# Performance work log

Hardware: AMD Instinct MI355X
Metric: run time of the kernel (lower is better)

Reference implementation:

```python
import jax, jax.numpy as jnp
import numpy as np

B, N, F, D, DB, C = 1024, 200000, 32, 128, 256, 96


def _ln(x, g, b, eps=1e-5):
    m = x.mean(-1, keepdims=True)
    v = ((x - m) ** 2).mean(-1, keepdims=True)
    return (x - m) / jnp.sqrt(v + eps) * g + b


def setup_inputs() -> dict:
    key = jax.random.key(0)
    ks = jax.random.split(key, 24)
    s = 0.05
    inp = {
        'x_num': jax.random.normal(ks[0], (B, F), jnp.float32),
        'cand_x_num': jax.random.normal(ks[1], (N, F), jnp.float32),
        'cand_y': jax.random.normal(ks[2], (N,), jnp.float32),
        'W_in': jax.random.normal(ks[3], (F, D), jnp.float32) * s,
        'b_in': jnp.zeros((D,), jnp.float32),
        'enc_w1': jax.random.normal(ks[4], (D, DB), jnp.float32) * s,
        'enc_b1': jnp.zeros((DB,), jnp.float32),
        'enc_w2': jax.random.normal(ks[5], (DB, D), jnp.float32) * s,
        'enc_b2': jnp.zeros((D,), jnp.float32),
        'ln_mix_g': jnp.ones((D,), jnp.float32),
        'ln_mix_b': jnp.zeros((D,), jnp.float32),
        'K_w': jax.random.normal(ks[6], (D, D), jnp.float32) * s,
        'K_b': jnp.zeros((D,), jnp.float32),
        'lab_w': jax.random.normal(ks[7], (1, D), jnp.float32) * s,
        'lab_b': jnp.zeros((D,), jnp.float32),
        'T_w1': jax.random.normal(ks[8], (D, DB), jnp.float32) * s,
        'T_b1': jnp.zeros((DB,), jnp.float32),
        'T_w2': jax.random.normal(ks[9], (DB, D), jnp.float32) * s,  # no bias
        'pred_ln_g': jnp.ones((D,), jnp.float32),
        'pred_ln_b': jnp.zeros((D,), jnp.float32),
        'pred_w1': jax.random.normal(ks[10], (D, DB), jnp.float32) * s,
        'pred_b1': jnp.zeros((DB,), jnp.float32),
        'pred_w2': jax.random.normal(ks[11], (DB, D), jnp.float32) * s,
        'pred_b2': jnp.zeros((D,), jnp.float32),
        'head_ln_g': jnp.ones((D,), jnp.float32),
        'head_ln_b': jnp.zeros((D,), jnp.float32),
        'head_w': jax.random.normal(ks[12], (D, 1), jnp.float32) * s,
        'head_b': jnp.zeros((1,), jnp.float32),
        'context_size': C,
    }
    return inp


def _forward(x_num, cand_x_num, cand_y, W_in, b_in, enc_w1, enc_b1, enc_w2, enc_b2,
             ln_mix_g, ln_mix_b, K_w, K_b, lab_w, lab_b, T_w1, T_b1, T_w2,
             pred_ln_g, pred_ln_b, pred_w1, pred_b1, pred_w2, pred_b2,
             head_ln_g, head_ln_b, head_w, head_b, context_size):
    def enc(z):
        h = z @ W_in + b_in                                   # [*, D]
        h = h + (jax.nn.relu(h @ enc_w1 + enc_b1) @ enc_w2 + enc_b2)
        k = _ln(h, ln_mix_g, ln_mix_b) @ K_w + K_b
        return h, k

    cand_k = enc(cand_x_num)[1]                               # [N, D]
    x, k = enc(x_num)                                         # [B, D]

    # brute-force kNN: negative squared L2 via matmul + square sums
    k2 = (k * k).sum(-1, keepdims=True)                       # [B, 1]
    ck2 = (cand_k * cand_k).sum(-1)                           # [N]
    sims = 2.0 * (k @ cand_k.T) - k2 - ck2[None, :]           # [B, N]
    _, idx = jax.lax.top_k(sims, context_size)                # [B, C]

    context_k = cand_k[idx]                                   # [B, C, D]
    sim_c = 2.0 * jnp.einsum('bd,bcd->bc', k, context_k) - k2 - (context_k ** 2).sum(-1)
    probs = jax.nn.softmax(sim_c, axis=-1)                    # [B, C]

    ctx_y = cand_y[idx][..., None] @ lab_w + lab_b            # [B, C, D]
    diff = k[:, None, :] - context_k                          # [B, C, D]
    vals = ctx_y + jax.nn.relu(diff @ T_w1 + T_b1) @ T_w2     # [B, C, D]
    context_x = jnp.einsum('bc,bcd->bd', probs, vals)         # [B, D]

    x = x + context_x
    h = _ln(x, pred_ln_g, pred_ln_b)
    x = x + (jax.nn.relu(h @ pred_w1 + pred_b1) @ pred_w2 + pred_b2)
    out = jax.nn.relu(_ln(x, head_ln_g, head_ln_b)) @ head_w + head_b
    return out                                                # [B, 1]


def reference(x_num, cand_x_num, cand_y, W_in, b_in, enc_w1, enc_b1, enc_w2, enc_b2,
              ln_mix_g, ln_mix_b, K_w, K_b, lab_w, lab_b, T_w1, T_b1, T_w2,
              pred_ln_g, pred_ln_b, pred_w1, pred_b1, pred_w2, pred_b2,
              head_ln_g, head_ln_b, head_w, head_b, context_size):
    return _forward(x_num, cand_x_num, cand_y, W_in, b_in, enc_w1, enc_b1, enc_w2, enc_b2,
                    ln_mix_g, ln_mix_b, K_w, K_b, lab_w, lab_b, T_w1, T_b1, T_w2,
                    pred_ln_g, pred_ln_b, pred_w1, pred_b1, pred_w2, pred_b2,
                    head_ln_g, head_ln_b, head_w, head_b, context_size)
```

## Files before the change

kernel.cpp:

```cpp
#include <hip/hip_runtime.h>
#include <hip/hip_bf16.h>

#define NC 200000
#define NCP 200064
#define NCT 1563
#define CGR 196
#define BB 1024
#define DD 128
#define DBH 256
#define CS 96
#define CAPS 8192
#define RSLOT6 6

typedef __attribute__((ext_vector_type(8))) short bf16x8;
typedef __attribute__((ext_vector_type(4))) float f32x4;

#define LDH 136
#define LDU 264
#define LDT 136

__device__ inline uint4 pack8(const float4 a, const float4 b) {
  union { __hip_bfloat16 h[8]; uint4 v; } r;
  r.h[0] = __float2bfloat16(a.x); r.h[1] = __float2bfloat16(a.y);
  r.h[2] = __float2bfloat16(a.z); r.h[3] = __float2bfloat16(a.w);
  r.h[4] = __float2bfloat16(b.x); r.h[5] = __float2bfloat16(b.y);
  r.h[6] = __float2bfloat16(b.z); r.h[7] = __float2bfloat16(b.w);
  return r.v;
}

__device__ inline unsigned encf(float v) {
  unsigned b = __float_as_uint(v);
  return (b & 0x80000000u) ? ~b : (b | 0x80000000u);
}
__device__ inline float decf(unsigned u) {
  return __uint_as_float((u & 0x80000000u) ? (u ^ 0x80000000u) : ~u);
}
__device__ inline unsigned long long mkkey(float v, int idx) {
  unsigned u = encf(v);
  return (((unsigned long long)(~u)) << 32) | (unsigned)idx;
}

__global__ __launch_bounds__(256) void k_prep(const float* __restrict__ w1,
                                              const float* __restrict__ w2,
                                              const float* __restrict__ kw,
                                              const float* __restrict__ tw1,
                                              __hip_bfloat16* __restrict__ w1t,
                                              __hip_bfloat16* __restrict__ w2t,
                                              __hip_bfloat16* __restrict__ kwt,
                                              __hip_bfloat16* __restrict__ tw1t) {
  const int i = blockIdx.x * 256 + threadIdx.x;
  if (i < 32768) {
    const int u = i >> 7, j = i & 127;
    w1t[i] = __float2bfloat16(w1[j * DBH + u]);
    tw1t[i] = __float2bfloat16(tw1[j * DBH + u]);
  }
  if (i < 32768) {
    const int d = i >> 8, u = i & 255;
    w2t[i] = __float2bfloat16(w2[u * DD + d]);
  }
  if (i < 16384) {
    const int d = i >> 7, j = i & 127;
    kwt[i] = __float2bfloat16(kw[j * DD + d]);
  }
}

__global__ __launch_bounds__(256) void k_pad(__hip_bfloat16* __restrict__ ckb16,
                                             float* __restrict__ ck2) {
  const int i = blockIdx.x * 256 + threadIdx.x;
  if (i < (NCP - NC) * DD) ckb16[(size_t)NC * DD + i] = __float2bfloat16(0.f);
  if (i < (NCP - NC)) ck2[NC + i] = 1e9f;
}

__global__ __launch_bounds__(256) void k_clear(unsigned* __restrict__ rowmaxP,
                                               int* __restrict__ cnt) {
  const int i = blockIdx.x * 256 + threadIdx.x;
  if (i < BB * 16) { rowmaxP[i] = 0u; cnt[i] = 0; }
}

__global__ __launch_bounds__(256) void k_e1(const float* __restrict__ X,
                                            const float* __restrict__ W,
                                            const float* __restrict__ bias,
                                            float* __restrict__ H) {
  __shared__ float Xs[32 * 32];
  const int tid = threadIdx.x;
  const int r0 = blockIdx.x * 32;
  ((float4*)Xs)[tid] = ((const float4*)(X + (size_t)r0 * 32))[tid];
  __syncthreads();
  const int d0 = tid & 63;
  const int rh = tid >> 6;
  float acc0[8], acc1[8];
  const float b0 = bias[d0], b1 = bias[d0 + 64];
#pragma unroll
  for (int r = 0; r < 8; ++r) { acc0[r] = b0; acc1[r] = b1; }
#pragma unroll
  for (int k4 = 0; k4 < 8; ++k4) {
    float w0[4], w1[4];
#pragma unroll
    for (int kk = 0; kk < 4; ++kk) {
      w0[kk] = W[(k4 * 4 + kk) * DD + d0];
      w1[kk] = W[(k4 * 4 + kk) * DD + d0 + 64];
    }
#pragma unroll
    for (int r = 0; r < 8; ++r) {
      float4 x4 = ((const float4*)(Xs + (rh * 8 + r) * 32))[k4];
      acc0[r] += x4.x * w0[0] + x4.y * w0[1] + x4.z * w0[2] + x4.w * w0[3];
      acc1[r] += x4.x * w1[0] + x4.y * w1[1] + x4.z * w1[2] + x4.w * w1[3];
    }
  }
#pragma unroll
  for (int r = 0; r < 8; ++r) {
    const size_t row = (size_t)(r0 + rh * 8 + r);
    H[row * DD + d0] = acc0[r];
    H[row * DD + d0 + 64] = acc1[r];
  }
}

__global__ __launch_bounds__(256) void k_e23m(float* __restrict__ H,
                                              const __hip_bfloat16* __restrict__ W1t,
                                              const float* __restrict__ B1,
                                              const __hip_bfloat16* __restrict__ W2t,
                                              const float* __restrict__ B2) {
  __shared__ __hip_bfloat16 Hs[64 * LDH];
  __shared__ __hip_bfloat16 Us[64 * LDU];
  const int tid = threadIdx.x;
  const int r0 = blockIdx.x * 64;
#pragma unroll
  for (int i = 0; i < 4; ++i) {
    const int e8 = i * 256 + tid;
    const int row = e8 >> 4, c8 = e8 & 15;
    const float* src = H + (size_t)(r0 + row) * DD + c8 * 8;
    float4 f0 = *(const float4*)(src);
    float4 f1 = *(const float4*)(src + 4);
    *(uint4*)(Hs + row * LDH + c8 * 8) = pack8(f0, f1);
  }
  __syncthreads();
  const int l = tid & 63, w = tid >> 6;
  const int lr = l & 15, lg = l >> 4;
  {
    f32x4 acc[4][4] = {};
#pragma unroll
    for (int kk = 0; kk < 4; ++kk) {
      bf16x8 a[4], b[4];
#pragma unroll
      for (int mi = 0; mi < 4; ++mi)
        a[mi] = *(const bf16x8*)(Hs + (mi * 16 + lr) * LDH + kk * 32 + lg * 8);
#pragma unroll
      for (int ni = 0; ni < 4; ++ni)
        b[ni] = *(const bf16x8*)(W1t + (size_t)(w * 64 + ni * 16 + lr) * DD + kk * 32 + lg * 8);
#pragma unroll
      for (int mi = 0; mi < 4; ++mi)
#pragma unroll
        for (int ni = 0; ni < 4; ++ni)
          acc[mi][ni] = __builtin_amdgcn_mfma_f32_16x16x32_bf16(a[mi], b[ni], acc[mi][ni], 0, 0, 0);
    }
#pragma unroll
    for (int ni = 0; ni < 4; ++ni) {
      const int col = w * 64 + ni * 16 + lr;
      const float bb = B1[col];
#pragma unroll
      for (int mi = 0; mi < 4; ++mi)
#pragma unroll
        for (int r = 0; r < 4; ++r) {
          const int row = mi * 16 + lg * 4 + r;
          Us[row * LDU + col] = __float2bfloat16(fmaxf(acc[mi][ni][r] + bb, 0.f));
        }
    }
  }
  __syncthreads();
  {
    f32x4 acc[4][2] = {};
#pragma unroll
    for (int kk = 0; kk < 8; ++kk) {
      bf16x8 a[4], b[2];
#pragma unroll
      for (int mi = 0; mi < 4; ++mi)
        a[mi] = *(const bf16x8*)(Us + (mi * 16 + lr) * LDU + kk * 32 + lg * 8);
#pragma unroll
      for (int ni = 0; ni < 2; ++ni)
        b[ni] = *(const bf16x8*)(W2t + (size_t)(w * 32 + ni * 16 + lr) * DBH + kk * 32 + lg * 8);
#pragma unroll
      for (int mi = 0; mi < 4; ++mi)
#pragma unroll
        for (int ni = 0; ni < 2; ++ni)
          acc[mi][ni] = __builtin_amdgcn_mfma_f32_16x16x32_bf16(a[mi], b[ni], acc[mi][ni], 0, 0, 0);
    }
#pragma unroll
    for (int ni = 0; ni < 2; ++ni) {
      const int col = w * 32 + ni * 16 + lr;
      const float bb = B2[col];
#pragma unroll
      for (int mi = 0; mi < 4; ++mi)
#pragma unroll
        for (int r = 0; r < 4; ++r) {
          const int row = mi * 16 + lg * 4 + r;
          const size_t g = (size_t)(r0 + row) * DD + col;
          H[g] = H[g] + acc[mi][ni][r] + bb;
        }
    }
  }
}

__global__ __launch_bounds__(256) void k_e4m(const float* __restrict__ H,
                                             const float* __restrict__ g,
                                             const float* __restrict__ bln,
                                             const __hip_bfloat16* __restrict__ Kwt,
                                             const float* __restrict__ Kb,
                                             float* __restrict__ Kout,
                                             __hip_bfloat16* __restrict__ Kb16,
                                             float* __restrict__ k2out) {
  __shared__ __hip_bfloat16 Ls[64 * LDH];
  __shared__ float k2s[64];
  const int tid = threadIdx.x;
  const int r0 = blockIdx.x * 64;
  if (tid < 64) k2s[tid] = 0.f;
  {
    const int row = tid >> 2, q = tid & 3;
    const float* hr = H + (size_t)(r0 + row) * DD + q * 32;
    float v[32];
#pragma unroll
    for (int i = 0; i < 8; ++i) {
      float4 f = ((const float4*)hr)[i];
      v[i * 4 + 0] = f.x; v[i * 4 + 1] = f.y; v[i * 4 + 2] = f.z; v[i * 4 + 3] = f.w;
    }
    float s = 0.f;
#pragma unroll
    for (int i = 0; i < 32; ++i) s += v[i];
    s += __shfl_xor(s, 1); s += __shfl_xor(s, 2);
    const float mean = s * (1.f / 128.f);
    float vs = 0.f;
#pragma unroll
    for (int i = 0; i < 32; ++i) { float d = v[i] - mean; vs += d * d; }
    vs += __shfl_xor(vs, 1); vs += __shfl_xor(vs, 2);
    const float rstd = 1.f / sqrtf(vs * (1.f / 128.f) + 1e-5f);
#pragma unroll
    for (int i = 0; i < 4; ++i) {
      float t[8];
#pragma unroll
      for (int j = 0; j < 8; ++j) {
        const int col = q * 32 + i * 8 + j;
        t[j] = (v[i * 8 + j] - mean) * rstd * g[col] + bln[col];
      }
      float4 f0 = {t[0], t[1], t[2], t[3]}, f1 = {t[4], t[5], t[6], t[7]};
      *(uint4*)(Ls + row * LDH + q * 32 + i * 8) = pack8(f0, f1);
    }
  }
  __syncthreads();
  const int l = tid & 63, w = tid >> 6;
  const int lr = l & 15, lg = l >> 4;
  f32x4 acc[4][2] = {};
#pragma unroll
  for (int kk = 0; kk < 4; ++kk) {
    bf16x8 a[4], b[2];
#pragma unroll
    for (int mi = 0; mi < 4; ++mi)
      a[mi] = *(const bf16x8*)(Ls + (mi * 16 + lr) * LDH + kk * 32 + lg * 8);
#pragma unroll
    for (int ni = 0; ni < 2; ++ni)
      b[ni] = *(const bf16x8*)(Kwt + (size_t)(w * 32 + ni * 16 + lr) * DD + kk * 32 + lg * 8);
#pragma unroll
    for (int mi = 0; mi < 4; ++mi)
#pragma unroll
      for (int ni = 0; ni < 2; ++ni)
        acc[mi][ni] = __builtin_amdgcn_mfma_f32_16x16x32_bf16(a[mi], b[ni], acc[mi][ni], 0, 0, 0);
  }
  float p[4][4];
#pragma unroll
  for (int mi = 0; mi < 4; ++mi)
#pragma unroll
    for (int r = 0; r < 4; ++r) p[mi][r] = 0.f;
#pragma unroll
  for (int ni = 0; ni < 2; ++ni) {
    const int col = w * 32 + ni * 16 + lr;
    const float kb = Kb[col];
#pragma unroll
    for (int mi = 0; mi < 4; ++mi)
#pragma unroll
      for (int r = 0; r < 4; ++r) {
        const float val = acc[mi][ni][r] + kb;
        const int row = mi * 16 + lg * 4 + r;
        const size_t gg = (size_t)(r0 + row) * DD + col;
        Kout[gg] = val;
        Kb16[gg] = __float2bfloat16(val);
        p[mi][r] += val * val;
      }
  }
#pragma unroll
  for (int mi = 0; mi < 4; ++mi)
#pragma unroll
    for (int r = 0; r < 4; ++r) {
      float t = p[mi][r];
      t += __shfl_xor(t, 1); t += __shfl_xor(t, 2);
      t += __shfl_xor(t, 4); t += __shfl_xor(t, 8);
      if (lr == 0) atomicAdd(&k2s[mi * 16 + lg * 4 + r], t);
    }
  __syncthreads();
  if (tid < 64) k2out[r0 + tid] = k2s[tid];
}

__global__ __launch_bounds__(256) void k_simsA(const __hip_bfloat16* __restrict__ A,
                                               const __hip_bfloat16* __restrict__ Bm,
                                               const float* __restrict__ ck2,
                                               unsigned* __restrict__ rowmaxP) {
  __shared__ __hip_bfloat16 As[128 * LDT];
  __shared__ __hip_bfloat16 Bs[128 * LDT];
  __shared__ float ck2s[128];
  __shared__ unsigned rmax_s[128];
  const int tid = threadIdx.x;
  const int bid = blockIdx.x;
  const int gq = bid >> 6, rem = bid & 63;
  const int rt = rem >> 3, xq = rem & 7;
  const int ct = gq * 8 + xq;
  if (ct >= NCT) return;
  const int m0 = rt * 128, n0 = ct * 128;
  if (tid < 128) { rmax_s[tid] = 0u; ck2s[tid] = 0.5f * ck2[n0 + tid]; }
  {
    const uint4* ga = (const uint4*)(A + (size_t)m0 * DD);
    const uint4* gb = (const uint4*)(Bm + (size_t)n0 * DD);
#pragma unroll
    for (int i = 0; i < 8; ++i) {
      const int e8 = i * 256 + tid;
      const int row = e8 >> 4, c8 = e8 & 15;
      *(uint4*)(As + row * LDT + c8 * 8) = ga[e8];
      *(uint4*)(Bs + row * LDT + c8 * 8) = gb[e8];
    }
  }
  __syncthreads();
  const int l = tid & 63, w = tid >> 6;
  const int wm = w >> 1, wn = w & 1;
  const int lr = l & 15, lg = l >> 4;
  f32x4 acc[4][4] = {};
#pragma unroll
  for (int kk = 0; kk < 4; ++kk) {
    bf16x8 a[4], b[4];
#pragma unroll
    for (int mi = 0; mi < 4; ++mi)
      a[mi] = *(const bf16x8*)(As + (wm * 64 + mi * 16 + lr) * LDT + kk * 32 + lg * 8);
#pragma unroll
    for (int ni = 0; ni < 4; ++ni)
      b[ni] = *(const bf16x8*)(Bs + (wn * 64 + ni * 16 + lr) * LDT + kk * 32 + lg * 8);
#pragma unroll
    for (int mi = 0; mi < 4; ++mi)
#pragma unroll
      for (int ni = 0; ni < 4; ++ni)
        acc[mi][ni] = __builtin_amdgcn_mfma_f32_16x16x32_bf16(a[mi], b[ni], acc[mi][ni], 0, 0, 0);
  }
  float vmax[4][4];
#pragma unroll
  for (int mi = 0; mi < 4; ++mi)
#pragma unroll
    for (int r = 0; r < 4; ++r) vmax[mi][r] = -1e30f;
#pragma unroll
  for (int ni = 0; ni < 4; ++ni) {
    const float c2 = ck2s[wn * 64 + ni * 16 + lr];
#pragma unroll
    for (int mi = 0; mi < 4; ++mi)
#pragma unroll
      for (int r = 0; r < 4; ++r)
        vmax[mi][r] = fmaxf(vmax[mi][r], acc[mi][ni][r] - c2);
  }
#pragma unroll
  for (int mi = 0; mi < 4; ++mi)
#pragma unroll
    for (int r = 0; r < 4; ++r) {
      float v = vmax[mi][r];
#pragma unroll
      for (int mk = 1; mk < 16; mk <<= 1) v = fmaxf(v, __shfl_xor(v, mk));
      if (lr == 0) atomicMax(&rmax_s[wm * 64 + mi * 16 + lg * 4 + r], encf(v));
    }
  __syncthreads();
  if (tid < 128) atomicMax(&rowmaxP[(m0 + tid) * 16], rmax_s[tid]);
}

__global__ __launch_bounds__(256) void k_simsB(const __hip_bfloat16* __restrict__ A,
                                               const __hip_bfloat16* __restrict__ Bm,
                                               const float* __restrict__ ck2,
                                               const unsigned* __restrict__ rowmaxP,
                                               unsigned long long* __restrict__ cand,
                                               int* __restrict__ cnt) {
  __shared__ __hip_bfloat16 As[128 * LDT];
  __shared__ __hip_bfloat16 Bs[128 * LDT];
  __shared__ float ck2s[128];
  __shared__ float cut_s[128];
  __shared__ unsigned long long loc[128][RSLOT6];
  __shared__ int lcnt[128];
  __shared__ int lbase[128];
  const int tid = threadIdx.x;
  const int bid = blockIdx.x;
  const int gq = bid >> 6, rem = bid & 63;
  const int rt = rem >> 3, xq = rem & 7;
  const int ct = gq * 8 + xq;
  if (ct >= NCT) return;
  const int m0 = rt * 128, n0 = ct * 128;
  if (tid < 128) {
    ck2s[tid] = 0.5f * ck2[n0 + tid];
    const float t = decf(rowmaxP[(m0 + tid) * 16]) - 7.0f;
    cut_s[tid] = t - (fabsf(t) + 8.0f) * 0.00390625f - 1e-5f;
    lcnt[tid] = 0;
  }
  {
    const uint4* ga = (const uint4*)(A + (size_t)m0 * DD);
    const uint4* gb = (const uint4*)(Bm + (size_t)n0 * DD);
#pragma unroll
    for (int i = 0; i < 8; ++i) {
      const int e8 = i * 256 + tid;
      const int row = e8 >> 4, c8 = e8 & 15;
      *(uint4*)(As + row * LDT + c8 * 8) = ga[e8];
      *(uint4*)(Bs + row * LDT + c8 * 8) = gb[e8];
    }
  }
  __syncthreads();
  const int l = tid & 63, w = tid >> 6;
  const int wm = w >> 1, wn = w & 1;
  const int lr = l & 15, lg = l >> 4;
  f32x4 acc[4][4] = {};
#pragma unroll
  for (int kk = 0; kk < 4; ++kk) {
    bf16x8 a[4], b[4];
#pragma unroll
    for (int mi = 0; mi < 4; ++mi)
      a[mi] = *(const bf16x8*)(As + (wm * 64 + mi * 16 + lr) * LDT + kk * 32 + lg * 8);
#pragma unroll
    for (int ni = 0; ni < 4; ++ni)
      b[ni] = *(const bf16x8*)(Bs + (wn * 64 + ni * 16 + lr) * LDT + kk * 32 + lg * 8);
#pragma unroll
    for (int mi = 0; mi < 4; ++mi)
#pragma unroll
      for (int ni = 0; ni < 4; ++ni)
        acc[mi][ni] = __builtin_amdgcn_mfma_f32_16x16x32_bf16(a[mi], b[ni], acc[mi][ni], 0, 0, 0);
  }
#pragma unroll
  for (int ni = 0; ni < 4; ++ni) {
    const int lcol = wn * 64 + ni * 16 + lr;
    const float c2 = ck2s[lcol];
    const int gcol = n0 + lcol;
#pragma unroll
    for (int mi = 0; mi < 4; ++mi)
#pragma unroll
      for (int r = 0; r < 4; ++r) {
        const int lrow = wm * 64 + mi * 16 + lg * 4 + r;
        const float x = acc[mi][ni][r] - c2;
        if (x >= cut_s[lrow]) {
          const float v = __bfloat162float(__float2bfloat16(x));
          const unsigned long long key = mkkey(v, gcol);
          const int q = atomicAdd(&lcnt[lrow], 1);
          if (q < RSLOT6) {
            loc[lrow][q] = key;
          } else {
            const int q2 = atomicAdd(&cnt[(m0 + lrow) * 16], 1);
            if (q2 < CAPS) cand[(size_t)(m0 + lrow) * CAPS + q2] = key;
          }
        }
      }
  }
  __syncthreads();
  if (tid < 128) {
    const int nres = lcnt[tid] < RSLOT6 ? lcnt[tid] : RSLOT6;
    lbase[tid] = atomicAdd(&cnt[(m0 + tid) * 16], nres);
  }
  __syncthreads();
  for (int e = tid; e < 128 * RSLOT6; e += 256) {
    const int rr = e / RSLOT6, s = e % RSLOT6;
    const int nres = lcnt[rr] < RSLOT6 ? lcnt[rr] : RSLOT6;
    if (s < nres) {
      const int pos = lbase[rr] + s;
      if (pos < CAPS) cand[(size_t)(m0 + rr) * CAPS + pos] = loc[rr][s];
    }
  }
}

__global__ __launch_bounds__(256) void k_sortB(const unsigned long long* __restrict__ cand,
                                               const int* __restrict__ cnt,
                                               int* __restrict__ idx_out) {
  __shared__ int wred[40][4];
  __shared__ int outl[128];
  __shared__ int outc_sh;
  const int tid = threadIdx.x;
  const int wid = tid >> 6, lane = tid & 63;
  const int row = blockIdx.x;
  int n = cnt[row * 16];
  if (n > CAPS) n = CAPS;

  unsigned v16l[32];
  int idl[32];
  {
    const unsigned long long* src = cand + (size_t)row * CAPS;
#pragma unroll
    for (int s = 0; s < 32; ++s) {
      const int i = tid + s * 256;
      if (i < n) {
        const unsigned long long k = src[i];
        v16l[s] = (~(unsigned)(k >> 32)) >> 16;
        idl[s] = (int)(k & 0xFFFFFFFFu);
      } else {
        v16l[s] = 0u;
        idl[s] = 0x7FFFFFFF;
      }
    }
  }

  int pass = 0;
  unsigned prefix = 0;
  int need = CS;
#pragma unroll
  for (int b = 15; b >= 0; --b) {
    int c1 = 0;
#pragma unroll
    for (int s = 0; s < 32; ++s)
      c1 += ((v16l[s] >> (b + 1)) == prefix && ((v16l[s] >> b) & 1u)) ? 1 : 0;
#pragma unroll
    for (int d = 1; d < 64; d <<= 1) c1 += __shfl_xor(c1, d);
    if (lane == 0) wred[pass][wid] = c1;
    __syncthreads();
    const int cnt1 = wred[pass][0] + wred[pass][1] + wred[pass][2] + wred[pass][3];
    ++pass;
    if (need <= cnt1) prefix = (prefix << 1) | 1u;
    else { need -= cnt1; prefix = (prefix << 1); }
  }
  const unsigned V16star = prefix;

  unsigned iprefix = 0;
  int ineed = need;
#pragma unroll
  for (int b = 17; b >= 0; --b) {
    int c0 = 0;
#pragma unroll
    for (int s = 0; s < 32; ++s)
      c0 += (v16l[s] == V16star && ((unsigned)idl[s] >> (b + 1)) == iprefix &&
             !(((unsigned)idl[s] >> b) & 1u)) ? 1 : 0;
#pragma unroll
    for (int d = 1; d < 64; d <<= 1) c0 += __shfl_xor(c0, d);
    if (lane == 0) wred[pass][wid] = c0;
    __syncthreads();
    const int cnt0 = wred[pass][0] + wred[pass][1] + wred[pass][2] + wred[pass][3];
    ++pass;
    if (ineed <= cnt0) iprefix = (iprefix << 1);
    else { ineed -= cnt0; iprefix = (iprefix << 1) | 1u; }
  }
  const unsigned ITstar = iprefix;

  if (tid == 0) outc_sh = 0;
  __syncthreads();
#pragma unroll
  for (int s = 0; s < 32; ++s) {
    if (v16l[s] > V16star || (v16l[s] == V16star && (unsigned)idl[s] <= ITstar)) {
      const int q = atomicAdd(&outc_sh, 1);
      if (q < 128) outl[q] = idl[s];
    }
  }
  __syncthreads();
  const int ne = outc_sh;
  for (int i = tid; i < 128; i += 256)
    if (i >= ne) outl[i] = 0x7FFFFFFF;
  __syncthreads();
  for (int k = 2; k <= 128; k <<= 1) {
    for (int j = k >> 1; j > 0; j >>= 1) {
      if (tid < 128) {
        const int i = tid, ixj = i ^ j;
        if (ixj > i) {
          int a = outl[i], b = outl[ixj];
          const bool up = ((i & k) == 0);
          if ((a > b) == up) { outl[i] = b; outl[ixj] = a; }
        }
      }
      __syncthreads();
    }
  }
  if (tid < CS) {
    int id = outl[tid];
    if ((unsigned)id >= NC) id = 0;
    idx_out[row * CS + tid] = id;
  }
}

#define LDB 136
__global__ __launch_bounds__(256) void k_final(const float* __restrict__ XH,
                                               const float* __restrict__ XK,
                                               const float* __restrict__ CK,
                                               const float* __restrict__ CY,
                                               const int* __restrict__ IDX,
                                               const __hip_bfloat16* __restrict__ Tw1t,
                                               const float* __restrict__ Tb1,
                                               const float* __restrict__ Tw2,
                                               const float* __restrict__ labw,
                                               const float* __restrict__ labb,
                                               const float* __restrict__ pg,
                                               const float* __restrict__ pb,
                                               const float* __restrict__ pw1,
                                               const float* __restrict__ pb1,
                                               const float* __restrict__ pw2,
                                               const float* __restrict__ pb2,
                                               const float* __restrict__ hg,
                                               const float* __restrict__ hb,
                                               const float* __restrict__ hw,
                                               const float* __restrict__ hbias,
                                               float* __restrict__ OUT) {
  __shared__ float diffs[CS * 132];
  __shared__ int ids[CS];
  __shared__ float yv[CS], simc[CS], pr[CS];
  __shared__ float kv[DD], xv[DD];
  __shared__ float qs[DBH];
  __shared__ float xrow[DD], hln[DD], t2[DBH], x2[DD];
  __shared__ float red[DD];
  __shared__ float smv[1];
  const int tid = threadIdx.x;
  const int b = blockIdx.x;
  if (tid < CS) ids[tid] = IDX[b * CS + tid];
  if (tid < DD) { kv[tid] = XK[(size_t)b * DD + tid]; xv[tid] = XH[(size_t)b * DD + tid]; }
  __syncthreads();
  if (tid < CS) yv[tid] = CY[ids[tid]];
  for (int e = tid; e < CS * DD; e += 256) {
    const int c = e >> 7, j = e & 127;
    diffs[c * 132 + j] = kv[j] - CK[(size_t)ids[c] * DD + j];
  }
  __syncthreads();
  if (tid < CS) {
    float s = 0.f;
    for (int j = 0; j < DD; ++j) { float d = diffs[tid * 132 + j]; s -= d * d; }
    simc[tid] = s;
  }
  __syncthreads();
  if (tid < DD) red[tid] = (tid < CS) ? simc[tid] : -1e30f;
  __syncthreads();
  for (int s = 64; s > 0; s >>= 1) { if (tid < s) red[tid] = fmaxf(red[tid], red[tid + s]); __syncthreads(); }
  const float mx = red[0];
  __syncthreads();
  if (tid < DD) red[tid] = (tid < CS) ? expf(simc[tid] - mx) : 0.f;
  if (tid < CS) pr[tid] = expf(simc[tid] - mx);
  __syncthreads();
  for (int s = 64; s > 0; s >>= 1) { if (tid < s) red[tid] += red[tid + s]; __syncthreads(); }
  const float inv = 1.f / red[0];
  __syncthreads();
  if (tid < CS) pr[tid] *= inv;
  if (tid < DD) red[tid] = (tid < CS) ? pr[tid] * yv[tid] : 0.f;
  __syncthreads();
  for (int s = 64; s > 0; s >>= 1) { if (tid < s) red[tid] += red[tid + s]; __syncthreads(); }
  if (tid == 0) smv[0] = red[0];
  __hip_bfloat16* db16 = (__hip_bfloat16*)diffs;
  {
    float4 f0s[6], f1s[6];
#pragma unroll
    for (int i = 0; i < 6; ++i) {
      const int gidx = tid + 256 * i;
      const int row = gidx >> 4, c8 = gidx & 15;
      f0s[i] = *(const float4*)(diffs + row * 132 + c8 * 8);
      f1s[i] = *(const float4*)(diffs + row * 132 + c8 * 8 + 4);
    }
    __syncthreads();
#pragma unroll
    for (int i = 0; i < 6; ++i) {
      const int gidx = tid + 256 * i;
      const int row = gidx >> 4, c8 = gidx & 15;
      *(uint4*)(db16 + row * LDB + c8 * 8) = pack8(f0s[i], f1s[i]);
    }
  }
  __syncthreads();
  {
    const int w = tid >> 6, l = tid & 63;
    const int lr = l & 15, lg = l >> 4;
    const int u0 = w * 64;
    bf16x8 af[6][4];
#pragma unroll
    for (int mt = 0; mt < 6; ++mt)
#pragma unroll
      for (int k = 0; k < 4; ++k)
        af[mt][k] = *(const bf16x8*)(db16 + (mt * 16 + lr) * LDB + k * 32 + lg * 8);
#pragma unroll
    for (int nt = 0; nt < 4; ++nt) {
      const int u = u0 + nt * 16 + lr;
      bf16x8 bfr[4];
#pragma unroll
      for (int k = 0; k < 4; ++k)
        bfr[k] = *(const bf16x8*)(Tw1t + (size_t)u * DD + k * 32 + lg * 8);
      const float bb = Tb1[u];
      float qacc = 0.f;
#pragma unroll
      for (int mt = 0; mt < 6; ++mt) {
        f32x4 acc = {};
#pragma unroll
        for (int k = 0; k < 4; ++k)
          acc = __builtin_amdgcn_mfma_f32_16x16x32_bf16(af[mt][k], bfr[k], acc, 0, 0, 0);
#pragma unroll
        for (int r = 0; r < 4; ++r) {
          const int c = mt * 16 + lg * 4 + r;
          qacc += pr[c] * fmaxf(acc[r] + bb, 0.f);
        }
      }
      qacc += __shfl_xor(qacc, 16);
      qacc += __shfl_xor(qacc, 32);
      if (lg == 0) qs[u] = qacc;
    }
  }
  __syncthreads();
  if (tid < DD) {
    const int d = tid;
    float cx = smv[0] * labw[d] + labb[d];
    for (int u4 = 0; u4 < 64; ++u4) {
      float4 q4 = *(const float4*)(&qs[u4 * 4]);
      cx += q4.x * Tw2[(u4 * 4 + 0) * DD + d];
      cx += q4.y * Tw2[(u4 * 4 + 1) * DD + d];
      cx += q4.z * Tw2[(u4 * 4 + 2) * DD + d];
      cx += q4.w * Tw2[(u4 * 4 + 3) * DD + d];
    }
    xrow[d] = xv[d] + cx;
  }
  __syncthreads();
  if (tid < DD) red[tid] = xrow[tid];
  __syncthreads();
  for (int s = 64; s > 0; s >>= 1) { if (tid < s) red[tid] += red[tid + s]; __syncthreads(); }
  const float m1 = red[0] * (1.f / 128.f);
  __syncthreads();
  if (tid < DD) { float d = xrow[tid] - m1; red[tid] = d * d; }
  __syncthreads();
  for (int s = 64; s > 0; s >>= 1) { if (tid < s) red[tid] += red[tid + s]; __syncthreads(); }
  const float rstd1 = 1.f / sqrtf(red[0] * (1.f / 128.f) + 1e-5f);
  __syncthreads();
  if (tid < DD) hln[tid] = (xrow[tid] - m1) * rstd1 * pg[tid] + pb[tid];
  __syncthreads();
  {
    const int u = tid;
    float s = pb1[u];
    for (int j4 = 0; j4 < 32; ++j4) {
      float4 h4 = *(const float4*)(hln + j4 * 4);
      s += h4.x * pw1[(j4 * 4 + 0) * DBH + u];
      s += h4.y * pw1[(j4 * 4 + 1) * DBH + u];
      s += h4.z * pw1[(j4 * 4 + 2) * DBH + u];
      s += h4.w * pw1[(j4 * 4 + 3) * DBH + u];
    }
    t2[u] = fmaxf(s, 0.f);
  }
  __syncthreads();
  if (tid < DD) {
    const int d = tid;
    float s = pb2[d];
    for (int u4 = 0; u4 < 64; ++u4) {
      float4 t4 = *(const float4*)(t2 + u4 * 4);
      s += t4.x * pw2[(u4 * 4 + 0) * DD + d];
      s += t4.y * pw2[(u4 * 4 + 1) * DD + d];
      s += t4.z * pw2[(u4 * 4 + 2) * DD + d];
      s += t4.w * pw2[(u4 * 4 + 3) * DD + d];
    }
    x2[d] = xrow[d] + s;
  }
  __syncthreads();
  if (tid < DD) red[tid] = x2[tid];
  __syncthreads();
  for (int s = 64; s > 0; s >>= 1) { if (tid < s) red[tid] += red[tid + s]; __syncthreads(); }
  const float m2 = red[0] * (1.f / 128.f);
  __syncthreads();
  if (tid < DD) { float d = x2[tid] - m2; red[tid] = d * d; }
  __syncthreads();
  for (int s = 64; s > 0; s >>= 1) { if (tid < s) red[tid] += red[tid + s]; __syncthreads(); }
  const float rstd2 = 1.f / sqrtf(red[0] * (1.f / 128.f) + 1e-5f);
  __syncthreads();
  if (tid < DD) {
    float z = (x2[tid] - m2) * rstd2 * hg[tid] + hb[tid];
    z = fmaxf(z, 0.f);
    red[tid] = z * hw[tid];
  }
  __syncthreads();
  for (int s = 64; s > 0; s >>= 1) { if (tid < s) red[tid] += red[tid + s]; __syncthreads(); }
  if (tid == 0) OUT[b] = red[0] + hbias[0];
}

extern "C" void kernel_launch(void* const* d_in, const int* in_sizes, int n_in,
                              void* d_out, int out_size, void* d_ws, size_t ws_size,
                              hipStream_t stream) {
  (void)in_sizes; (void)n_in; (void)out_size; (void)ws_size;
  const float* x_num      = (const float*)d_in[0];
  const float* cand_x     = (const float*)d_in[1];
  const float* cand_y     = (const float*)d_in[2];
  const float* W_in       = (const float*)d_in[3];
  const float* b_in       = (const float*)d_in[4];
  const float* enc_w1     = (const float*)d_in[5];
  const float* enc_b1     = (const float*)d_in[6];
  const float* enc_w2     = (const float*)d_in[7];
  const float* enc_b2     = (const float*)d_in[8];
  const float* ln_mix_g   = (const float*)d_in[9];
  const float* ln_mix_b   = (const float*)d_in[10];
  const float* K_w        = (const float*)d_in[11];
  const float* K_b        = (const float*)d_in[12];
  const float* lab_w      = (const float*)d_in[13];
  const float* lab_b      = (const float*)d_in[14];
  const float* T_w1       = (const float*)d_in[15];
  const float* T_b1       = (const float*)d_in[16];
  const float* T_w2       = (const float*)d_in[17];
  const float* pred_ln_g  = (const float*)d_in[18];
  const float* pred_ln_b  = (const float*)d_in[19];
  const float* pred_w1    = (const float*)d_in[20];
  const float* pred_b1    = (const float*)d_in[21];
  const float* pred_w2    = (const float*)d_in[22];
  const float* pred_b2    = (const float*)d_in[23];
  const float* head_ln_g  = (const float*)d_in[24];
  const float* head_ln_b  = (const float*)d_in[25];
  const float* head_w     = (const float*)d_in[26];
  const float* head_b     = (const float*)d_in[27];
  float* out = (float*)d_out;

  char* w8 = (char*)d_ws;
  size_t off = 0;
  float* cand_k = (float*)(w8 + off);              off += (size_t)NC * DD * 4;
  float* cand_ck2 = (float*)(w8 + off);            off += (size_t)NCP * 4 + 256;
  float* xh = (float*)(w8 + off);                  off += (size_t)BB * DD * 4;
  float* xk = (float*)(w8 + off);                  off += (size_t)BB * DD * 4;
  float* xk2 = (float*)(w8 + off);                 off += 4096;
  __hip_bfloat16* xkb16 = (__hip_bfloat16*)(w8 + off); off += (size_t)BB * DD * 2;
  int* idx_all = (int*)(w8 + off);                 off += (size_t)BB * CS * 4;
  __hip_bfloat16* w1t = (__hip_bfloat16*)(w8 + off); off += (size_t)DBH * DD * 2;
  __hip_bfloat16* w2t = (__hip_bfloat16*)(w8 + off); off += (size_t)DD * DBH * 2;
  __hip_bfloat16* kwt = (__hip_bfloat16*)(w8 + off); off += (size_t)DD * DD * 2;
  __hip_bfloat16* tw1t = (__hip_bfloat16*)(w8 + off); off += (size_t)DBH * DD * 2;
  unsigned* rowmaxP = (unsigned*)(w8 + off);       off += (size_t)BB * 16 * 4;
  int* cntb = (int*)(w8 + off);                    off += (size_t)BB * 16 * 4;
  char* big = w8 + off;
  float* cand_h = (float*)big;
  unsigned long long* candb = (unsigned long long*)big;
  __hip_bfloat16* ckb16 = (__hip_bfloat16*)(big + (size_t)NC * DD * 4);

  k_prep<<<128, 256, 0, stream>>>(enc_w1, enc_w2, K_w, T_w1, w1t, w2t, kwt, tw1t);
  k_pad<<<32, 256, 0, stream>>>(ckb16, cand_ck2);
  k_e1<<<NC / 32, 256, 0, stream>>>(cand_x, W_in, b_in, cand_h);
  k_e23m<<<NC / 64, 256, 0, stream>>>(cand_h, w1t, enc_b1, w2t, enc_b2);
  k_e4m<<<NC / 64, 256, 0, stream>>>(cand_h, ln_mix_g, ln_mix_b, kwt, K_b,
                                     cand_k, ckb16, cand_ck2);
  k_e1<<<BB / 32, 256, 0, stream>>>(x_num, W_in, b_in, xh);
  k_e23m<<<BB / 64, 256, 0, stream>>>(xh, w1t, enc_b1, w2t, enc_b2);
  k_e4m<<<BB / 64, 256, 0, stream>>>(xh, ln_mix_g, ln_mix_b, kwt, K_b,
                                     xk, xkb16, xk2);
  k_clear<<<64, 256, 0, stream>>>(rowmaxP, cntb);
  k_simsA<<<CGR * 64, 256, 0, stream>>>(xkb16, ckb16, cand_ck2, rowmaxP);
  k_simsB<<<CGR * 64, 256, 0, stream>>>(xkb16, ckb16, cand_ck2, rowmaxP, candb, cntb);
  k_sortB<<<BB, 256, 0, stream>>>(candb, cntb, idx_all);
  k_final<<<BB, 256, 0, stream>>>(xh, xk, cand_k, cand_y, idx_all,
                                  tw1t, T_b1, T_w2, lab_w, lab_b,
                                  pred_ln_g, pred_ln_b, pred_w1, pred_b1, pred_w2, pred_b2,
                                  head_ln_g, head_ln_b, head_w, head_b, out);
}
```

Measured before the change: 668.1 us.

## Loop over all query row tiles per candidate block in similarity kernels

Both similarity kernels now launch one block per 128-candidate column tile and loop over all 8 query row tiles inside the block. The candidate tile is staged in LDS once, and query fragments are read straight from global memory into registers. This removes the repeated B-tile loads and launch overhead of 8x more blocks, and cuts global atomics on the row max to one per row per block. In exchange there are fewer, longer blocks (1563, which may leave the GPU unevenly loaded), more per-iteration syncs, unstaged global A reads, and local candidate slots grow from 6 to 8.

```diff
diff --git a/kernel.cpp b/kernel.cpp
--- a/kernel.cpp
+++ b/kernel.cpp
@@ -4,13 +4,12 @@
 #define NC 200000
 #define NCP 200064
 #define NCT 1563
-#define CGR 196
 #define BB 1024
 #define DD 128
 #define DBH 256
 #define CS 96
 #define CAPS 8192
-#define RSLOT6 6
+#define RSLOT 8
 
 typedef __attribute__((ext_vector_type(8))) short bf16x8;
 typedef __attribute__((ext_vector_type(4))) float f32x4;
@@ -301,26 +300,20 @@
                                                const __hip_bfloat16* __restrict__ Bm,
                                                const float* __restrict__ ck2,
                                                unsigned* __restrict__ rowmaxP) {
-  __shared__ __hip_bfloat16 As[128 * LDT];
   __shared__ __hip_bfloat16 Bs[128 * LDT];
   __shared__ float ck2s[128];
-  __shared__ unsigned rmax_s[128];
+  __shared__ unsigned rmax_s[BB];
   const int tid = threadIdx.x;
-  const int bid = blockIdx.x;
-  const int gq = bid >> 6, rem = bid & 63;
-  const int rt = rem >> 3, xq = rem & 7;
-  const int ct = gq * 8 + xq;
-  if (ct >= NCT) return;
-  const int m0 = rt * 128, n0 = ct * 128;
-  if (tid < 128) { rmax_s[tid] = 0u; ck2s[tid] = 0.5f * ck2[n0 + tid]; }
+  const int n0 = blockIdx.x * 128;
+#pragma unroll
+  for (int i = 0; i < 4; ++i) rmax_s[i * 256 + tid] = 0u;
+  if (tid < 128) ck2s[tid] = 0.5f * ck2[n0 + tid];
   {
-    const uint4* ga = (const uint4*)(A + (size_t)m0 * DD);
     const uint4* gb = (const uint4*)(Bm + (size_t)n0 * DD);
 #pragma unroll
     for (int i = 0; i < 8; ++i) {
       const int e8 = i * 256 + tid;
       const int row = e8 >> 4, c8 = e8 & 15;
-      *(uint4*)(As + row * LDT + c8 * 8) = ga[e8];
       *(uint4*)(Bs + row * LDT + c8 * 8) = gb[e8];
     }
   }
@@ -328,47 +321,51 @@
   const int l = tid & 63, w = tid >> 6;
   const int wm = w >> 1, wn = w & 1;
   const int lr = l & 15, lg = l >> 4;
-  f32x4 acc[4][4] = {};
-#pragma unroll
-  for (int kk = 0; kk < 4; ++kk) {
-    bf16x8 a[4], b[4];
+  float c2l[4];
+#pragma unroll
+  for (int ni = 0; ni < 4; ++ni) c2l[ni] = ck2s[wn * 64 + ni * 16 + lr];
+  for (int rt = 0; rt < 8; ++rt) {
+    const int m0 = rt * 128;
+    bf16x8 a[4][4];
+#pragma unroll
+    for (int mi = 0; mi < 4; ++mi) {
+      const __hip_bfloat16* ar = A + (size_t)(m0 + wm * 64 + mi * 16 + lr) * DD + lg * 8;
+#pragma unroll
+      for (int kk = 0; kk < 4; ++kk) a[mi][kk] = *(const bf16x8*)(ar + kk * 32);
+    }
+    f32x4 acc[4][4] = {};
+#pragma unroll
+    for (int kk = 0; kk < 4; ++kk) {
+      bf16x8 b[4];
+#pragma unroll
+      for (int ni = 0; ni < 4; ++ni)
+        b[ni] = *(const bf16x8*)(Bs + (wn * 64 + ni * 16 + lr) * LDT + kk * 32 + lg * 8);
+#pragma unroll
+      for (int mi = 0; mi < 4; ++mi)
+#pragma unroll
+        for (int ni = 0; ni < 4; ++ni)
+          acc[mi][ni] = __builtin_amdgcn_mfma_f32_16x16x32_bf16(a[mi][kk], b[ni], acc[mi][ni], 0, 0, 0);
+    }
 #pragma unroll
     for (int mi = 0; mi < 4; ++mi)
-      a[mi] = *(const bf16x8*)(As + (wm * 64 + mi * 16 + lr) * LDT + kk * 32 + lg * 8);
-#pragma unroll
-    for (int ni = 0; ni < 4; ++ni)
-      b[ni] = *(const bf16x8*)(Bs + (wn * 64 + ni * 16 + lr) * LDT + kk * 32 + lg * 8);
-#pragma unroll
-    for (int mi = 0; mi < 4; ++mi)
-#pragma unroll
-      for (int ni = 0; ni < 4; ++ni)
-        acc[mi][ni] = __builtin_amdgcn_mfma_f32_16x16x32_bf16(a[mi], b[ni], acc[mi][ni], 0, 0, 0);
-  }
-  float vmax[4][4];
-#pragma unroll
-  for (int mi = 0; mi < 4; ++mi)
-#pragma unroll
-    for (int r = 0; r < 4; ++r) vmax[mi][r] = -1e30f;
-#pragma unroll
-  for (int ni = 0; ni < 4; ++ni) {
-    const float c2 = ck2s[wn * 64 + ni * 16 + lr];
-#pragma unroll
-    for (int mi = 0; mi < 4; ++mi)
-#pragma unroll
-      for (int r = 0; r < 4; ++r)
-        vmax[mi][r] = fmaxf(vmax[mi][r], acc[mi][ni][r] - c2);
-  }
-#pragma unroll
-  for (int mi = 0; mi < 4; ++mi)
-#pragma unroll
-    for (int r = 0; r < 4; ++r) {
-      float v = vmax[mi][r];
-#pragma unroll
-      for (int mk = 1; mk < 16; mk <<= 1) v = fmaxf(v, __shfl_xor(v, mk));
-      if (lr == 0) atomicMax(&rmax_s[wm * 64 + mi * 16 + lg * 4 + r], encf(v));
-    }
-  __syncthreads();
-  if (tid < 128) atomicMax(&rowmaxP[(m0 + tid) * 16], rmax_s[tid]);
+#pragma unroll
+      for (int r = 0; r < 4; ++r) {
+        float v = -1e30f;
+#pragma unroll
+        for (int ni = 0; ni < 4; ++ni) v = fmaxf(v, acc[mi][ni][r] - c2l[ni]);
+#pragma unroll
+        for (int mk = 1; mk < 16; mk <<= 1) v = fmaxf(v, __shfl_xor(v, mk));
+        if (lr == 0)
+          atomicMax(&rmax_s[m0 + wm * 64 + mi * 16 + lg * 4 + r], encf(v));
+      }
+  }
+  __syncthreads();
+#pragma unroll
+  for (int i = 0; i < 4; ++i) {
+    const int row = i * 256 + tid;
+    const unsigned e = rmax_s[row];
+    if (e) atomicMax(&rowmaxP[row * 16], e);
+  }
 }
 
 __global__ __launch_bounds__(256) void k_simsB(const __hip_bfloat16* __restrict__ A,
@@ -377,94 +374,102 @@
                                                const unsigned* __restrict__ rowmaxP,
                                                unsigned long long* __restrict__ cand,
                                                int* __restrict__ cnt) {
-  __shared__ __hip_bfloat16 As[128 * LDT];
   __shared__ __hip_bfloat16 Bs[128 * LDT];
   __shared__ float ck2s[128];
-  __shared__ float cut_s[128];
-  __shared__ unsigned long long loc[128][RSLOT6];
+  __shared__ float cut_all[BB];
+  __shared__ unsigned long long loc[128][RSLOT];
   __shared__ int lcnt[128];
   __shared__ int lbase[128];
   const int tid = threadIdx.x;
-  const int bid = blockIdx.x;
-  const int gq = bid >> 6, rem = bid & 63;
-  const int rt = rem >> 3, xq = rem & 7;
-  const int ct = gq * 8 + xq;
-  if (ct >= NCT) return;
-  const int m0 = rt * 128, n0 = ct * 128;
-  if (tid < 128) {
-    ck2s[tid] = 0.5f * ck2[n0 + tid];
-    const float t = decf(rowmaxP[(m0 + tid) * 16]) - 7.0f;
-    cut_s[tid] = t - (fabsf(t) + 8.0f) * 0.00390625f - 1e-5f;
-    lcnt[tid] = 0;
+  const int n0 = blockIdx.x * 128;
+  if (tid < 128) ck2s[tid] = 0.5f * ck2[n0 + tid];
+#pragma unroll
+  for (int i = 0; i < 4; ++i) {
+    const int row = i * 256 + tid;
+    const float t = decf(rowmaxP[row * 16]) - 7.0f;
+    cut_all[row] = t - (fabsf(t) + 8.0f) * 0.00390625f - 1e-5f;
   }
   {
-    const uint4* ga = (const uint4*)(A + (size_t)m0 * DD);
     const uint4* gb = (const uint4*)(Bm + (size_t)n0 * DD);
 #pragma unroll
     for (int i = 0; i < 8; ++i) {
       const int e8 = i * 256 + tid;
       const int row = e8 >> 4, c8 = e8 & 15;
-      *(uint4*)(As + row * LDT + c8 * 8) = ga[e8];
       *(uint4*)(Bs + row * LDT + c8 * 8) = gb[e8];
     }
   }
-  __syncthreads();
   const int l = tid & 63, w = tid >> 6;
   const int wm = w >> 1, wn = w & 1;
   const int lr = l & 15, lg = l >> 4;
-  f32x4 acc[4][4] = {};
-#pragma unroll
-  for (int kk = 0; kk < 4; ++kk) {
-    bf16x8 a[4], b[4];
-#pragma unroll
-    for (int mi = 0; mi < 4; ++mi)
-      a[mi] = *(const bf16x8*)(As + (wm * 64 + mi * 16 + lr) * LDT + kk * 32 + lg * 8);
-#pragma unroll
-    for (int ni = 0; ni < 4; ++ni)
-      b[ni] = *(const bf16x8*)(Bs + (wn * 64 + ni * 16 + lr) * LDT + kk * 32 + lg * 8);
-#pragma unroll
-    for (int mi = 0; mi < 4; ++mi)
+  float c2l[4];
+  int gcl[4];
+  __syncthreads();
+#pragma unroll
+  for (int ni = 0; ni < 4; ++ni) {
+    c2l[ni] = ck2s[wn * 64 + ni * 16 + lr];
+    gcl[ni] = n0 + wn * 64 + ni * 16 + lr;
+  }
+  for (int rt = 0; rt < 8; ++rt) {
+    const int m0 = rt * 128;
+    if (tid < 128) lcnt[tid] = 0;
+    __syncthreads();
+    bf16x8 a[4][4];
+#pragma unroll
+    for (int mi = 0; mi < 4; ++mi) {
+      const __hip_bfloat16* ar = A + (size_t)(m0 + wm * 64 + mi * 16 + lr) * DD + lg * 8;
+#pragma unroll
+      for (int kk = 0; kk < 4; ++kk) a[mi][kk] = *(const bf16x8*)(ar + kk * 32);
+    }
+    f32x4 acc[4][4] = {};
+#pragma unroll
+    for (int kk = 0; kk < 4; ++kk) {
+      bf16x8 b[4];
 #pragma unroll
       for (int ni = 0; ni < 4; ++ni)
-        acc[mi][ni] = __builtin_amdgcn_mfma_f32_16x16x32_bf16(a[mi], b[ni], acc[mi][ni], 0, 0, 0);
-  }
-#pragma unroll
-  for (int ni = 0; ni < 4; ++ni) {
-    const int lcol = wn * 64 + ni * 16 + lr;
-    const float c2 = ck2s[lcol];
-    const int gcol = n0 + lcol;
+        b[ni] = *(const bf16x8*)(Bs + (wn * 64 + ni * 16 + lr) * LDT + kk * 32 + lg * 8);
+#pragma unroll
+      for (int mi = 0; mi < 4; ++mi)
+#pragma unroll
+        for (int ni = 0; ni < 4; ++ni)
+          acc[mi][ni] = __builtin_amdgcn_mfma_f32_16x16x32_bf16(a[mi][kk], b[ni], acc[mi][ni], 0, 0, 0);
+    }
 #pragma unroll
     for (int mi = 0; mi < 4; ++mi)
 #pragma unroll
       for (int r = 0; r < 4; ++r) {
         const int lrow = wm * 64 + mi * 16 + lg * 4 + r;
-        const float x = acc[mi][ni][r] - c2;
-        if (x >= cut_s[lrow]) {
-          const float v = __bfloat162float(__float2bfloat16(x));
-          const unsigned long long key = mkkey(v, gcol);
-          const int q = atomicAdd(&lcnt[lrow], 1);
-          if (q < RSLOT6) {
-            loc[lrow][q] = key;
-          } else {
-            const int q2 = atomicAdd(&cnt[(m0 + lrow) * 16], 1);
-            if (q2 < CAPS) cand[(size_t)(m0 + lrow) * CAPS + q2] = key;
+        const float cut = cut_all[m0 + lrow];
+#pragma unroll
+        for (int ni = 0; ni < 4; ++ni) {
+          const float x = acc[mi][ni][r] - c2l[ni];
+          if (x >= cut) {
+            const float v = __bfloat162float(__float2bfloat16(x));
+            const unsigned long long key = mkkey(v, gcl[ni]);
+            const int q = atomicAdd(&lcnt[lrow], 1);
+            if (q < RSLOT) {
+              loc[lrow][q] = key;
+            } else {
+              const int q2 = atomicAdd(&cnt[(m0 + lrow) * 16], 1);
+              if (q2 < CAPS) cand[(size_t)(m0 + lrow) * CAPS + q2] = key;
+            }
           }
         }
       }
-  }
-  __syncthreads();
-  if (tid < 128) {
-    const int nres = lcnt[tid] < RSLOT6 ? lcnt[tid] : RSLOT6;
-    lbase[tid] = atomicAdd(&cnt[(m0 + tid) * 16], nres);
-  }
-  __syncthreads();
-  for (int e = tid; e < 128 * RSLOT6; e += 256) {
-    const int rr = e / RSLOT6, s = e % RSLOT6;
-    const int nres = lcnt[rr] < RSLOT6 ? lcnt[rr] : RSLOT6;
-    if (s < nres) {
-      const int pos = lbase[rr] + s;
-      if (pos < CAPS) cand[(size_t)(m0 + rr) * CAPS + pos] = loc[rr][s];
-    }
+    __syncthreads();
+    if (tid < 128) {
+      const int nres = lcnt[tid] < RSLOT ? lcnt[tid] : RSLOT;
+      lbase[tid] = nres ? atomicAdd(&cnt[(m0 + tid) * 16], nres) : 0;
+    }
+    __syncthreads();
+    for (int e = tid; e < 128 * RSLOT; e += 256) {
+      const int rr = e >> 3, s = e & (RSLOT - 1);
+      const int nres = lcnt[rr] < RSLOT ? lcnt[rr] : RSLOT;
+      if (s < nres) {
+        const int pos = lbase[rr] + s;
+        if (pos < CAPS) cand[(size_t)(m0 + rr) * CAPS + pos] = loc[rr][s];
+      }
+    }
+    __syncthreads();
   }
 }
 
@@ -827,8 +832,8 @@
   k_e4m<<<BB / 64, 256, 0, stream>>>(xh, ln_mix_g, ln_mix_b, kwt, K_b,
                                      xk, xkb16, xk2);
   k_clear<<<64, 256, 0, stream>>>(rowmaxP, cntb);
-  k_simsA<<<CGR * 64, 256, 0, stream>>>(xkb16, ckb16, cand_ck2, rowmaxP);
-  k_simsB<<<CGR * 64, 256, 0, stream>>>(xkb16, ckb16, cand_ck2, rowmaxP, candb, cntb);
+  k_simsA<<<NCT, 256, 0, stream>>>(xkb16, ckb16, cand_ck2, rowmaxP);
+  k_simsB<<<NCT, 256, 0, stream>>>(xkb16, ckb16, cand_ck2, rowmaxP, candb, cntb);
   k_sortB<<<BB, 256, 0, stream>>>(candb, cntb, idx_all);
   k_final<<<BB, 256, 0, stream>>>(xh, xk, cand_k, cand_y, idx_all,
                                   tw1t, T_b1, T_w2, lab_w, lab_b,
```

Result: slower. 782.1 us (+17.1%).
